# Kernel tuning notes

Measured on AMD Instinct MI355X. Metric: run time of the kernel, lower is better.

The kernel has to match this reference:

```python
import jax, jax.numpy as jnp
import numpy as np

DIM = 128

def setup_inputs() -> dict:
    key = jax.random.key(0)
    k1, k2, k3, k4, k5, k6 = jax.random.split(key, 6)
    bs = 16
    n_nodes = 65536  # bs * 4096 nodes per graph
    n_edges = 500000
    node_features = jax.random.normal(k1, (n_nodes, DIM), dtype=jnp.float32)
    edge_index = jax.random.randint(k2, (2, n_edges), 0, n_nodes, dtype=jnp.int64)
    centroid = jax.random.normal(k3, (bs, DIM), dtype=jnp.float32)
    # MLP params: Linear(3*dim, dim) -> ReLU -> (Dropout eval=identity) -> Linear(dim, 1)
    lim1 = 1.0 / np.sqrt(3 * DIM)
    W1 = jax.random.uniform(k4, (3 * DIM, DIM), minval=-lim1, maxval=lim1, dtype=jnp.float32)
    b1 = jnp.zeros((DIM,), dtype=jnp.float32)
    lim2 = 1.0 / np.sqrt(DIM)
    W2 = jax.random.uniform(k5, (DIM, 1), minval=-lim2, maxval=lim2, dtype=jnp.float32)
    b2 = jnp.zeros((1,), dtype=jnp.float32)
    return {"node_features": node_features, "edge_index": edge_index, "centroid": centroid,
            "bs": bs, "W1": W1, "b1": b1, "W2": W2, "b2": b2}

def reference(node_features, edge_index, centroid, bs, W1, b1, W2, b2):
    # node_features: [N, dim]; edge_index: [2, E]; centroid: [bs, dim]
    nf = node_features.reshape(-1, DIM)
    node_j = nf[edge_index[0]]  # [E, dim]
    node_i = nf[edge_index[1]]  # [E, dim]
    # residual = node_features - per-graph centroid
    residual = (nf.reshape(bs, -1, DIM) - centroid.reshape(bs, 1, DIM)).reshape(-1, DIM)
    res_j = residual[edge_index[0]]
    res_i = residual[edge_index[1]]
    sim_vec = jnp.concatenate([jnp.abs(node_i - node_j), res_i, res_j], axis=1)  # [E, 3*dim]
    h = jax.nn.relu(sim_vec @ W1 + b1)  # dropout is identity in eval mode
    prob_score = h @ W2 + b2  # [E, 1]
    return prob_score
```

## Files before the change

kernel.cpp:

```cpp
#include <hip/hip_runtime.h>
#include <hip/hip_bf16.h>
#include <stdint.h>

#define DIM 128

typedef __attribute__((ext_vector_type(8))) short short8;
typedef __attribute__((ext_vector_type(4))) float f32x4;
typedef __attribute__((ext_vector_type(8))) unsigned short ushort8;

__device__ __forceinline__ float bf2f(unsigned short u) {
    unsigned int x = ((unsigned int)u) << 16;
    return __builtin_bit_cast(float, x);
}
__device__ __forceinline__ unsigned short f2bf(float f) {
    unsigned int x = __builtin_bit_cast(unsigned int, f);
    x += 0x7fffu + ((x >> 16) & 1u);
    return (unsigned short)(x >> 16);
}

__global__ void prep_weights(const float* __restrict__ W1,
                             unsigned short* __restrict__ W1bcT,
                             unsigned short* __restrict__ packA) {
    int t = blockIdx.x * 256 + threadIdx.x;
    if (t < 256 * 128) {
        int c = t >> 7, k = t & 127;
        int row = 128 + ((c >> 7) << 7) + k;
        W1bcT[t] = f2bf(W1[row * DIM + (c & 127)]);
    } else {
        int o = t - 256 * 128;
        int x = o & 7, l = (o >> 3) & 63, o2 = o >> 9;
        int s = o2 & 3, T = o2 >> 2;
        int col = T * 16 + (l & 15);
        int k = s * 32 + (l >> 4) * 8 + x;
        packA[o] = f2bf(W1[k * DIM + col]);
    }
}

__global__ __launch_bounds__(512) void precompute_PQ(
    const float* __restrict__ nf, const float* __restrict__ centroid,
    const unsigned short* __restrict__ W1bcT, const float* __restrict__ b1,
    unsigned short* __restrict__ nf16, unsigned short* __restrict__ PQ, int npg)
{
    __shared__ char sA[64 * 256];
    const int t = threadIdx.x;
    const int n0 = blockIdx.x * 64;

    {
        int row = t >> 3;
        int c0 = (t & 7) * 16;
        int n = n0 + row;
        int g = n / npg;
        const f32x4* nv = (const f32x4*)(nf + (size_t)n * DIM + c0);
        const f32x4* cv = (const f32x4*)(centroid + (size_t)g * DIM + c0);
        unsigned short sh[16];
        ushort8 raw[2];
#pragma unroll
        for (int u = 0; u < 4; ++u) {
            f32x4 a = nv[u], c = cv[u];
#pragma unroll
            for (int x = 0; x < 4; ++x) {
                raw[u >> 1][(u & 1) * 4 + x] = f2bf(a[x]);
                sh[u * 4 + x] = f2bf(a[x] - c[x]);
            }
        }
        *(ushort8*)(nf16 + (size_t)n * DIM + c0)     = raw[0];
        *(ushort8*)(nf16 + (size_t)n * DIM + c0 + 8) = raw[1];
#pragma unroll
        for (int v = 0; v < 2; ++v) {
            int inrow = c0 * 2 + v * 16;
            int phys = row * 256 + (inrow ^ ((row & 7) << 4));
            *(short8*)(sA + phys) = *(const short8*)(sh + v * 8);
        }
    }

    const int wid = t >> 6, l = t & 63, lo = l & 15, hi = l >> 4;
    const int wm = wid & 1, wn = wid >> 1;

    short8 B[4][4];
#pragma unroll
    for (int nt = 0; nt < 4; ++nt) {
        int row = wn * 64 + nt * 16 + lo;
        const short8* wp = (const short8*)(W1bcT + (size_t)row * DIM + hi * 8);
#pragma unroll
        for (int kk = 0; kk < 4; ++kk) B[nt][kk] = wp[kk * 4];
    }

    __syncthreads();

    f32x4 acc[2][4];
#pragma unroll
    for (int mt = 0; mt < 2; ++mt)
#pragma unroll
        for (int nt = 0; nt < 4; ++nt) acc[mt][nt] = (f32x4)0.0f;

#pragma unroll
    for (int kk = 0; kk < 4; ++kk) {
        short8 a[2];
#pragma unroll
        for (int mt = 0; mt < 2; ++mt) {
            int row = wm * 32 + mt * 16 + lo;
            int inrow = kk * 64 + hi * 16;
            int phys = row * 256 + (inrow ^ ((row & 7) << 4));
            a[mt] = *(const short8*)(sA + phys);
        }
#pragma unroll
        for (int mt = 0; mt < 2; ++mt)
#pragma unroll
            for (int nt = 0; nt < 4; ++nt)
                acc[mt][nt] = __builtin_amdgcn_mfma_f32_16x16x32_bf16(
                    a[mt], B[nt][kk], acc[mt][nt], 0, 0, 0);
    }

#pragma unroll
    for (int nt = 0; nt < 4; ++nt) {
        int col = wn * 64 + nt * 16 + lo;
        float bb = (col < DIM) ? b1[col] : 0.0f;
#pragma unroll
        for (int mt = 0; mt < 2; ++mt)
#pragma unroll
            for (int q = 0; q < 4; ++q) {
                int n = n0 + wm * 32 + mt * 16 + hi * 4 + q;
                PQ[(size_t)n * 256 + col] = f2bf(acc[mt][nt][q] + bb);
            }
    }
}

#define ITERS 4
__global__ __launch_bounds__(256, 6) void edge_kernel(
    const unsigned short* __restrict__ nf16, const int* __restrict__ idx,
    const unsigned short* __restrict__ PQ, const unsigned short* __restrict__ packA,
    const float* __restrict__ W2, const float* __restrict__ b2,
    float* __restrict__ out, int E, int nTiles)
{
    __shared__ char  sD[32 * 256];
    __shared__ float sS[32 * 132];
    __shared__ float sR[4][32];
    const int t = threadIdx.x;
    const int l = t & 63, wn = t >> 6, lo = l & 15, hi = l >> 4;

    short8 B[2][4];
    {
        const short8* bp = (const short8*)packA;
#pragma unroll
        for (int nt = 0; nt < 2; ++nt)
#pragma unroll
            for (int kk = 0; kk < 4; ++kk)
                B[nt][kk] = bp[((wn * 2 + nt) * 4 + kk) * 64 + l];
    }
    float w2v[2];
#pragma unroll
    for (int nt = 0; nt < 2; ++nt) w2v[nt] = W2[wn * 32 + nt * 16 + lo];
    const float b2v = b2[0];

    for (int it = 0; it < ITERS; ++it) {
        int tile = blockIdx.x * ITERS + it;
        if (tile >= nTiles) break;
        int e0 = tile * 32;

        {
            int e = t >> 3, c0 = (t & 7) * 16;
            int ge = e0 + e;
            int jj = 0, ii = 0;
            if (ge < E) { jj = idx[ge]; ii = idx[E + ge]; }
            const ushort8* pi = (const ushort8*)(nf16 + (size_t)ii * DIM + c0);
            const ushort8* pj = (const ushort8*)(nf16 + (size_t)jj * DIM + c0);
            const ushort8* Pp = (const ushort8*)(PQ + (size_t)ii * 256 + c0);
            const ushort8* Qp = (const ushort8*)(PQ + (size_t)jj * 256 + DIM + c0);
            ushort8 a0 = pi[0], a1 = pi[1], c0v = pj[0], c1v = pj[1];
            ushort8 P0 = Pp[0], P1 = Pp[1], Q0 = Qp[0], Q1 = Qp[1];
            unsigned short d[16];
            float s[16];
#pragma unroll
            for (int x = 0; x < 8; ++x) {
                d[x]     = f2bf(fabsf(bf2f(a0[x]) - bf2f(c0v[x])));
                d[8 + x] = f2bf(fabsf(bf2f(a1[x]) - bf2f(c1v[x])));
                s[x]     = bf2f(P0[x]) + bf2f(Q0[x]);
                s[8 + x] = bf2f(P1[x]) + bf2f(Q1[x]);
            }
            int rs = e * 256, sw = (e & 7) << 4, inb = c0 * 2;
            *(short8*)(sD + rs + ((inb     ) ^ sw)) = *(const short8*)d;
            *(short8*)(sD + rs + ((inb + 16) ^ sw)) = *(const short8*)(d + 8);
#pragma unroll
            for (int u = 0; u < 4; ++u)
                *(f32x4*)(sS + e * 132 + c0 + u * 4) = *(const f32x4*)(s + u * 4);
        }
        __syncthreads();

        f32x4 acc[2][2];
#pragma unroll
        for (int mt = 0; mt < 2; ++mt)
#pragma unroll
            for (int nt = 0; nt < 2; ++nt) acc[mt][nt] = (f32x4)0.0f;

#pragma unroll
        for (int kk = 0; kk < 4; ++kk) {
            short8 a[2];
#pragma unroll
            for (int mt = 0; mt < 2; ++mt) {
                int row = mt * 16 + lo;
                int inrow = kk * 64 + hi * 16;
                a[mt] = *(const short8*)(sD + row * 256 + (inrow ^ ((row & 7) << 4)));
            }
#pragma unroll
            for (int mt = 0; mt < 2; ++mt)
#pragma unroll
                for (int nt = 0; nt < 2; ++nt)
                    acc[mt][nt] = __builtin_amdgcn_mfma_f32_16x16x32_bf16(
                        a[mt], B[nt][kk], acc[mt][nt], 0, 0, 0);
        }

#pragma unroll
        for (int mt = 0; mt < 2; ++mt)
#pragma unroll
            for (int q = 0; q < 4; ++q) {
                int el = mt * 16 + hi * 4 + q;
                float s = 0.0f;
#pragma unroll
                for (int nt = 0; nt < 2; ++nt) {
                    int col = wn * 32 + nt * 16 + lo;
                    float h = acc[mt][nt][q] + sS[el * 132 + col];
                    s += fmaxf(h, 0.0f) * w2v[nt];
                }
                s += __shfl_xor(s, 1);
                s += __shfl_xor(s, 2);
                s += __shfl_xor(s, 4);
                s += __shfl_xor(s, 8);
                if (lo == 0) sR[wn][el] = s;
            }
        __syncthreads();
        if (t < 32) {
            int ge = e0 + t;
            if (ge < E)
                out[ge] = sR[0][t] + sR[1][t] + sR[2][t] + sR[3][t] + b2v;
        }
    }
}

extern "C" void kernel_launch(void* const* d_in, const int* in_sizes, int n_in,
                              void* d_out, int out_size, void* d_ws, size_t ws_size,
                              hipStream_t stream) {
    const float* nf       = (const float*)d_in[0];
    const int*   idx      = (const int*)d_in[1];
    const float* centroid = (const float*)d_in[2];
    const float* W1       = (const float*)d_in[4];
    const float* b1       = (const float*)d_in[5];
    const float* W2       = (const float*)d_in[6];
    const float* b2       = (const float*)d_in[7];
    float* out = (float*)d_out;

    const int n_nodes = in_sizes[0] / DIM;
    const int E       = in_sizes[1] / 2;
    const int bs      = in_sizes[2] / DIM;
    const int npg     = n_nodes / bs;

    unsigned short* nf16  = (unsigned short*)d_ws;
    unsigned short* PQ    = nf16 + (size_t)n_nodes * DIM;
    unsigned short* W1bcT = PQ + (size_t)n_nodes * 256;
    unsigned short* packA = W1bcT + 256 * 128;

    prep_weights<<<192, 256, 0, stream>>>(W1, W1bcT, packA);
    precompute_PQ<<<n_nodes / 64, 512, 0, stream>>>(nf, centroid, W1bcT, b1,
                                                    nf16, PQ, npg);
    int nTiles = (E + 31) / 32;
    edge_kernel<<<(nTiles + ITERS - 1) / ITERS, 256, 0, stream>>>(
        nf16, idx, PQ, packA, W2, b2, out, E, nTiles);
}
```

Measured before the change: 226.6 us.

## Software-pipeline edge gathers with register prefetch and longer per-block tile loop

The edge kernel now prefetches the next tile's gathered node and PQ rows into registers, and the index pair two tiles ahead, while the current tile runs its MFMA and reduction. This hides the random-gather latency behind compute. ITERS rises from 4 to 16 and the launch bound drops from 6 to 4 blocks per CU, which allows more registers for the prefetch buffers at the cost of fewer resident waves. The ge<E guard on idx loads was removed, so a tail tile past E could read out of bounds.

```diff
diff --git a/kernel.cpp b/kernel.cpp
--- a/kernel.cpp
+++ b/kernel.cpp
@@ -3,6 +3,7 @@
 #include <stdint.h>
 
 #define DIM 128
+#define ITERS 16
 
 typedef __attribute__((ext_vector_type(8))) short short8;
 typedef __attribute__((ext_vector_type(4))) float f32x4;
@@ -125,8 +126,29 @@
     }
 }
 
-#define ITERS 4
-__global__ __launch_bounds__(256, 6) void edge_kernel(
+__device__ __forceinline__ void stage_convert_write(
+    char* sD, float* sS, int e, int c0,
+    ushort8 a0, ushort8 a1, ushort8 b0, ushort8 b1,
+    ushort8 P0, ushort8 P1, ushort8 Q0, ushort8 Q1)
+{
+    unsigned short d[16];
+    float s[16];
+#pragma unroll
+    for (int x = 0; x < 8; ++x) {
+        d[x]     = f2bf(fabsf(bf2f(a0[x]) - bf2f(b0[x])));
+        d[8 + x] = f2bf(fabsf(bf2f(a1[x]) - bf2f(b1[x])));
+        s[x]     = bf2f(P0[x]) + bf2f(Q0[x]);
+        s[8 + x] = bf2f(P1[x]) + bf2f(Q1[x]);
+    }
+    int rs = e * 256, sw = (e & 7) << 4, inb = c0 * 2;
+    *(short8*)(sD + rs + ((inb     ) ^ sw)) = *(const short8*)d;
+    *(short8*)(sD + rs + ((inb + 16) ^ sw)) = *(const short8*)(d + 8);
+#pragma unroll
+    for (int u = 0; u < 4; ++u)
+        *(f32x4*)(sS + e * 132 + c0 + u * 4) = *(const f32x4*)(s + u * 4);
+}
+
+__global__ __launch_bounds__(256, 4) void edge_kernel(
     const unsigned short* __restrict__ nf16, const int* __restrict__ idx,
     const unsigned short* __restrict__ PQ, const unsigned short* __restrict__ packA,
     const float* __restrict__ W2, const float* __restrict__ b2,
@@ -137,6 +159,7 @@
     __shared__ float sR[4][32];
     const int t = threadIdx.x;
     const int l = t & 63, wn = t >> 6, lo = l & 15, hi = l >> 4;
+    const int es = t >> 3, c0 = (t & 7) * 16;
 
     short8 B[2][4];
     {
@@ -148,44 +171,42 @@
                 B[nt][kk] = bp[((wn * 2 + nt) * 4 + kk) * 64 + l];
     }
     float w2v[2];
-#pragma unroll
-    for (int nt = 0; nt < 2; ++nt) w2v[nt] = W2[wn * 32 + nt * 16 + lo];
+    w2v[0] = W2[wn * 32 + lo];
+    w2v[1] = W2[wn * 32 + 16 + lo];
     const float b2v = b2[0];
 
-    for (int it = 0; it < ITERS; ++it) {
-        int tile = blockIdx.x * ITERS + it;
-        if (tile >= nTiles) break;
-        int e0 = tile * 32;
-
-        {
-            int e = t >> 3, c0 = (t & 7) * 16;
-            int ge = e0 + e;
-            int jj = 0, ii = 0;
-            if (ge < E) { jj = idx[ge]; ii = idx[E + ge]; }
-            const ushort8* pi = (const ushort8*)(nf16 + (size_t)ii * DIM + c0);
-            const ushort8* pj = (const ushort8*)(nf16 + (size_t)jj * DIM + c0);
-            const ushort8* Pp = (const ushort8*)(PQ + (size_t)ii * 256 + c0);
-            const ushort8* Qp = (const ushort8*)(PQ + (size_t)jj * 256 + DIM + c0);
-            ushort8 a0 = pi[0], a1 = pi[1], c0v = pj[0], c1v = pj[1];
-            ushort8 P0 = Pp[0], P1 = Pp[1], Q0 = Qp[0], Q1 = Qp[1];
-            unsigned short d[16];
-            float s[16];
-#pragma unroll
-            for (int x = 0; x < 8; ++x) {
-                d[x]     = f2bf(fabsf(bf2f(a0[x]) - bf2f(c0v[x])));
-                d[8 + x] = f2bf(fabsf(bf2f(a1[x]) - bf2f(c1v[x])));
-                s[x]     = bf2f(P0[x]) + bf2f(Q0[x]);
-                s[8 + x] = bf2f(P1[x]) + bf2f(Q1[x]);
-            }
-            int rs = e * 256, sw = (e & 7) << 4, inb = c0 * 2;
-            *(short8*)(sD + rs + ((inb     ) ^ sw)) = *(const short8*)d;
-            *(short8*)(sD + rs + ((inb + 16) ^ sw)) = *(const short8*)(d + 8);
-#pragma unroll
-            for (int u = 0; u < 4; ++u)
-                *(f32x4*)(sS + e * 132 + c0 + u * 4) = *(const f32x4*)(s + u * 4);
-        }
-        __syncthreads();
-
+    const int tile0 = blockIdx.x * ITERS;
+    const int nT = min(ITERS, nTiles - tile0);
+
+    {
+        int ge = tile0 * 32 + es;
+        int jj = idx[ge], ii = idx[E + ge];
+        const ushort8* pi = (const ushort8*)(nf16 + (size_t)ii * DIM + c0);
+        const ushort8* pj = (const ushort8*)(nf16 + (size_t)jj * DIM + c0);
+        const ushort8* Pp = (const ushort8*)(PQ + (size_t)ii * 256 + c0);
+        const ushort8* Qp = (const ushort8*)(PQ + (size_t)jj * 256 + DIM + c0);
+        stage_convert_write(sD, sS, es, c0, pi[0], pi[1], pj[0], pj[1],
+                            Pp[0], Pp[1], Qp[0], Qp[1]);
+    }
+    ushort8 pA0, pA1, pB0, pB1, pP0, pP1, pQ0, pQ1;
+    int ii_n, jj_n;
+    {
+        int t1 = min(tile0 + 1, nTiles - 1);
+        int ge = t1 * 32 + es;
+        int jj = idx[ge], ii = idx[E + ge];
+        const ushort8* pi = (const ushort8*)(nf16 + (size_t)ii * DIM + c0);
+        const ushort8* pj = (const ushort8*)(nf16 + (size_t)jj * DIM + c0);
+        const ushort8* Pp = (const ushort8*)(PQ + (size_t)ii * 256 + c0);
+        const ushort8* Qp = (const ushort8*)(PQ + (size_t)jj * 256 + DIM + c0);
+        pA0 = pi[0]; pA1 = pi[1]; pB0 = pj[0]; pB1 = pj[1];
+        pP0 = Pp[0]; pP1 = Pp[1]; pQ0 = Qp[0]; pQ1 = Qp[1];
+        int t2 = min(tile0 + 2, nTiles - 1);
+        int ge2 = t2 * 32 + es;
+        jj_n = idx[ge2]; ii_n = idx[E + ge2];
+    }
+    __syncthreads();
+
+    for (int tt = 0; tt < nT; ++tt) {
         f32x4 acc[2][2];
 #pragma unroll
         for (int mt = 0; mt < 2; ++mt)
@@ -228,11 +249,31 @@
                 if (lo == 0) sR[wn][el] = s;
             }
         __syncthreads();
-        if (t < 32) {
-            int ge = e0 + t;
-            if (ge < E)
+
+        {
+            int ge = (tile0 + tt) * 32 + t;
+            if (t < 32 && ge < E)
                 out[ge] = sR[0][t] + sR[1][t] + sR[2][t] + sR[3][t] + b2v;
         }
+
+        if (tt + 1 < nT) {
+            stage_convert_write(sD, sS, es, c0, pA0, pA1, pB0, pB1,
+                                pP0, pP1, pQ0, pQ1);
+            {
+                const ushort8* pi = (const ushort8*)(nf16 + (size_t)ii_n * DIM + c0);
+                const ushort8* pj = (const ushort8*)(nf16 + (size_t)jj_n * DIM + c0);
+                const ushort8* Pp = (const ushort8*)(PQ + (size_t)ii_n * 256 + c0);
+                const ushort8* Qp = (const ushort8*)(PQ + (size_t)jj_n * 256 + DIM + c0);
+                pA0 = pi[0]; pA1 = pi[1]; pB0 = pj[0]; pB1 = pj[1];
+                pP0 = Pp[0]; pP1 = Pp[1]; pQ0 = Qp[0]; pQ1 = Qp[1];
+            }
+            {
+                int t3 = min(tile0 + tt + 3, nTiles - 1);
+                int ge3 = t3 * 32 + es;
+                jj_n = idx[ge3]; ii_n = idx[E + ge3];
+            }
+        }
+        __syncthreads();
     }
 }
 
```

Measured after the change: 185.8 us. 18.0% less time.
